# Kernel optimization log

Measured on AMD Instinct MI355X. Metric: run time of the kernel, lower is better.

The kernel has to match this reference:

```python
import jax, jax.numpy as jnp
import numpy as np
import math

N, C_IN, H, W = 8, 256, 64, 64
C_ATT, C_OUT = 128, 256
BN_EPS = 1e-5


def conv_bn_relu(x, w, gamma, beta, mean, var):
    # 1x1 conv (no bias) + BatchNorm (eval mode) + ReLU
    y = jnp.einsum('oc,nchw->nohw', w, x)
    inv = gamma / jnp.sqrt(var + BN_EPS)
    y = y * inv[None, :, None, None] + (beta - mean * inv)[None, :, None, None]
    return jax.nn.relu(y)


def setup_inputs() -> dict:
    key = jax.random.key(0)
    ks = jax.random.split(key, 12)
    x = jax.random.normal(ks[0], (N, C_IN, H, W), dtype=jnp.float32)
    mask = jnp.ones((N, 1, H, W), dtype=jnp.float32)
    reduc_w = jax.random.normal(ks[1], (C_OUT, C_IN), dtype=jnp.float32) * (1.0 / math.sqrt(C_IN))
    reduc_gamma = jnp.ones((C_OUT,), dtype=jnp.float32)
    reduc_beta = jnp.zeros((C_OUT,), dtype=jnp.float32)
    reduc_mean = jax.random.normal(ks[2], (C_OUT,), dtype=jnp.float32) * 0.1
    reduc_var = jax.random.uniform(ks[3], (C_OUT,), dtype=jnp.float32) + 0.5
    att_w = jax.random.normal(ks[4], (C_ATT, C_IN), dtype=jnp.float32) * (1.0 / math.sqrt(C_IN))
    att_gamma = jnp.ones((C_ATT,), dtype=jnp.float32)
    att_beta = jnp.zeros((C_ATT,), dtype=jnp.float32)
    att_mean = jax.random.normal(ks[5], (C_ATT,), dtype=jnp.float32) * 0.1
    att_var = jax.random.uniform(ks[6], (C_ATT,), dtype=jnp.float32) + 0.5
    return {
        'x': x, 'mask': mask,
        'reduc_w': reduc_w, 'reduc_gamma': reduc_gamma, 'reduc_beta': reduc_beta,
        'reduc_mean': reduc_mean, 'reduc_var': reduc_var,
        'att_w': att_w, 'att_gamma': att_gamma, 'att_beta': att_beta,
        'att_mean': att_mean, 'att_var': att_var,
    }


def reference(x, mask, reduc_w, reduc_gamma, reduc_beta, reduc_mean, reduc_var,
              att_w, att_gamma, att_beta, att_mean, att_var):
    n, _, h, w = x.shape
    x_feat = conv_bn_relu(x, reduc_w, reduc_gamma, reduc_beta, reduc_mean, reduc_var)   # [n,C_OUT,h,w]
    x_atten = conv_bn_relu(x, att_w, att_gamma, att_beta, att_mean, att_var)            # [n,C_ATT,h,w]
    c = x_atten.shape[1]
    q = x_atten.reshape(n, c, h * w)                                                    # [n,c,HW]
    # energy[n,i,j] = sum_c q[n,c,i]*q[n,c,j] / (1e-8 + sqrt(c))
    energy = jnp.einsum('nci,ncj->nij', q, q) / (1e-8 + math.sqrt(c))
    energy = energy + (mask.reshape(n, 1, h * w) - 1.0) * 1e8
    weight = jax.nn.softmax(energy, axis=2)                                             # [n,HW,HW]
    feat = x_feat.reshape(n, x_feat.shape[1], h * w)                                    # [n,C_OUT,HW]
    out = jnp.einsum('nij,ncj->nci', weight, feat)                                      # [n,C_OUT,HW]
    out = out.reshape(n, feat.shape[1], h, w)
    out = out * mask
    return out
```

## Files before the change

### kernel.cpp

```cpp
#include <hip/hip_runtime.h>
#include <cstdint>
#include <cstddef>

#define NB 8
#define CIN 256
#define HWX 4096
#define CF 256
#define CA 128
#define CT 384

typedef __attribute__((ext_vector_type(8))) _Float16 half8;
typedef __attribute__((ext_vector_type(8))) short short8;
typedef __attribute__((ext_vector_type(4))) float f32x4;
typedef __attribute__((ext_vector_type(4))) unsigned int u32x4;

#define OFF_WH   0
#define OFF_BIAS (CT*CIN*2)
#define OFF_FEAT (OFF_BIAS + CT*4)
#define OFF_Q    (OFF_FEAT + NB*CF*HWX*2)
#define OFF_NORM (OFF_Q + NB*HWX*CA*2)
#define OFF_G    (OFF_NORM + NB*HWX*4)

__device__ inline unsigned short f16_bits(float f) {
  _Float16 h = (_Float16)f;
  return __builtin_bit_cast(unsigned short, h);
}
__device__ inline half8 ld_half8(const unsigned short* p) {
  short8 r = *(const short8*)p;
  return __builtin_bit_cast(half8, r);
}

__device__ inline void g2l16(const void* g, void* l) {
  __builtin_amdgcn_global_load_lds(
      (const __attribute__((address_space(1))) unsigned int*)g,
      (__attribute__((address_space(3))) unsigned int*)l, 16, 0, 0);
}

__global__ __launch_bounds__(256) void fold_bn_k(
    const float* __restrict__ rw, const float* __restrict__ rg,
    const float* __restrict__ rb, const float* __restrict__ rm, const float* __restrict__ rv,
    const float* __restrict__ aw, const float* __restrict__ ag,
    const float* __restrict__ ab2, const float* __restrict__ am, const float* __restrict__ av,
    unsigned short* __restrict__ wh, float* __restrict__ bias, unsigned* __restrict__ Gmax) {
  int o = blockIdx.x, k = threadIdx.x;
  if (o == 0 && k < NB) Gmax[k] = 0u;
  const float* wsrc; float g, b, m, v;
  if (o < CF) { wsrc = rw + (size_t)o*CIN; g = rg[o]; b = rb[o]; m = rm[o]; v = rv[o]; }
  else { int oa = o - CF; wsrc = aw + (size_t)oa*CIN; g = ag[oa]; b = ab2[oa]; m = am[oa]; v = av[oa]; }
  float inv = g / sqrtf(v + 1e-5f);
  wh[(size_t)o*CIN + k] = f16_bits(wsrc[k] * inv);
  if (k == 0) bias[o] = b - m*inv;
}

__global__ __launch_bounds__(256, 2) void conv_k(
    const float* __restrict__ x, const unsigned short* __restrict__ wh,
    const float* __restrict__ bias, unsigned short* __restrict__ feat,
    unsigned short* __restrict__ q, float* __restrict__ normq,
    unsigned* __restrict__ Gmax) {
  __shared__ unsigned short sBuf[18432];
  __shared__ unsigned short sQr[64*136];
  int b = blockIdx.x;
  int n = b & 7, pt0 = b >> 3;
  int p0 = pt0 * 64;
  int t = threadIdx.x;
  int w = t >> 6, lane = t & 63, quad = lane >> 4, col = lane & 15;
  const float* xn = x + (size_t)n*CIN*HWX;

  #pragma unroll
  for (int pass=0; pass<8; pass++) {
    int idx = pass*256 + t;
    int kp = idx >> 4, pq = idx & 15;
    f32x4 a = *(const f32x4*)(xn + (size_t)(2*kp)*HWX + p0 + pq*4);
    f32x4 c = *(const f32x4*)(xn + (size_t)(2*kp+1)*HWX + p0 + pq*4);
    #pragma unroll
    for (int j=0;j<4;j++) {
      int pos = pq*4 + j;
      unsigned dd = (unsigned)f16_bits(a[j]) | ((unsigned)f16_bits(c[j]) << 16);
      *(unsigned*)&sBuf[pos*264 + kp*2] = dd;
    }
  }
  __syncthreads();

  f32x4 fzero = {0.f,0.f,0.f,0.f};
  f32x4 acc[4][6];
  #pragma unroll
  for (int pt=0;pt<4;pt++)
    #pragma unroll
    for (int ot=0;ot<6;ot++) acc[pt][ot] = fzero;

  #pragma unroll
  for (int ks=0; ks<8; ks++) {
    half8 B6[6];
    #pragma unroll
    for (int ot=0;ot<6;ot++)
      B6[ot] = ld_half8(wh + (size_t)(w*96 + ot*16 + col)*CIN + ks*32 + quad*8);
    half8 A4[4];
    #pragma unroll
    for (int pt=0;pt<4;pt++)
      A4[pt] = ld_half8(&sBuf[(pt*16+col)*264 + ks*32 + quad*8]);
    #pragma unroll
    for (int pt=0;pt<4;pt++)
      #pragma unroll
      for (int ot=0;ot<6;ot++)
        acc[pt][ot] = __builtin_amdgcn_mfma_f32_16x16x32_f16(A4[pt], B6[ot], acc[pt][ot], 0, 0, 0);
  }
  __syncthreads();

  float bv[6];
  #pragma unroll
  for (int ot=0;ot<6;ot++) bv[ot] = bias[w*96 + ot*16 + col];
  #pragma unroll
  for (int pt=0;pt<4;pt++)
    #pragma unroll
    for (int ot=0;ot<6;ot++) {
      int oc = w*96 + ot*16 + col;
      #pragma unroll
      for (int r=0;r<4;r++) {
        float v = fmaxf(acc[pt][ot][r] + bv[ot], 0.f);
        int pos = pt*16 + quad*4 + r;
        if (oc < CF) sBuf[oc*72 + pos] = f16_bits(v);
        else         sQr[pos*136 + (oc - CF)] = f16_bits(v);
      }
    }
  __syncthreads();

  {
    const unsigned short* src = &sBuf[t*72];
    unsigned short* dst = feat + (size_t)n*CF*HWX + (size_t)t*HWX + p0;
    #pragma unroll
    for (int s=0;s<8;s++)
      *(u32x4*)(dst + s*8) = *(const u32x4*)(src + s*8);
  }
  {
    int pos = t >> 2, seg = t & 3;
    const unsigned short* src = &sQr[pos*136 + seg*32];
    unsigned short* dst = q + ((size_t)n*HWX + p0 + pos)*CA + seg*32;
    float s2 = 0.f;
    #pragma unroll
    for (int u=0;u<4;u++) {
      short8 v = *(const short8*)(src + u*8);
      *(short8*)(dst + u*8) = v;
      half8 h = __builtin_bit_cast(half8, v);
      #pragma unroll
      for (int e=0;e<8;e++) { float fe = (float)h[e]; s2 += fe*fe; }
    }
    s2 += __shfl_xor(s2, 1, 64);
    s2 += __shfl_xor(s2, 2, 64);
    if (seg == 0) {
      float nv = sqrtf(s2);
      normq[(size_t)n*HWX + p0 + pos] = nv;
      atomicMax(Gmax + n, __float_as_uint(nv));
    }
  }
}

__global__ __launch_bounds__(512, 4) void flash_k(
    const unsigned short* __restrict__ q, const unsigned short* __restrict__ feat,
    const float* __restrict__ mask, const float* __restrict__ normq,
    const unsigned* __restrict__ Gmax, float* __restrict__ out) {
  __shared__ alignas(16) unsigned short sQ[64*128];
  __shared__ alignas(16) unsigned short sP[64][72];
  __shared__ float sM[64];
  __shared__ float sL[2][64];
  int b = blockIdx.x;
  int n = b & 7, it = b >> 3;
  int i0 = it * 64;
  int t = threadIdx.x;
  int w = t >> 6, lane = t & 63, quad = lane >> 4, col = lane & 15;
  int wq = w & 3, wh = w >> 2;
  const unsigned short* q_n = q + (size_t)n*HWX*CA;
  const unsigned short* f_n = feat + (size_t)n*CF*HWX;
  const float* m_n = mask + (size_t)n*HWX;
  const int rloc = (t >> 4) & 31, oct16 = t & 15;
  const float inv_s = 1.0f/(1e-8f + sqrtf(128.0f));

  auto stage_Q = [&](int j0) {
    #pragma unroll
    for (int c=0;c<2;c++) {
      int row = c*32 + rloc;
      int og = oct16 ^ (row & 15);
      g2l16(q_n + (size_t)(j0+row)*CA + og*8, &sQ[(size_t)row*128 + oct16*8]);
    }
    if (t < 16) g2l16(m_n + j0 + t*4, &sM[t*4]);
  };

  half8 ah[4];
  {
    int arow = i0 + wq*16 + col;
    #pragma unroll
    for (int ks=0; ks<4; ks++)
      ah[ks] = ld_half8(q_n + (size_t)arow*CA + ks*32 + quad*8);
  }
  float Gn = __uint_as_float(Gmax[n]);
  float cvals[4];
  #pragma unroll
  for (int r=0;r<4;r++)
    cvals[r] = normq[(size_t)n*HWX + i0 + wq*16 + quad*4 + r] * Gn * inv_s - 5.0f;

  f32x4 fzero = {0.f,0.f,0.f,0.f};
  f32x4 o[4][2];
  #pragma unroll
  for (int ig=0;ig<4;ig++) { o[ig][0] = fzero; o[ig][1] = fzero; }
  float lrun[4] = {0.f,0.f,0.f,0.f};

  stage_Q(0);
  for (int ji = 0; ji < 64; ji++) {
    int j0 = ji*64;
    __syncthreads();

    half8 bF[2][2];
    #pragma unroll
    for (int ks2=0;ks2<2;ks2++)
      #pragma unroll
      for (int ct=0;ct<2;ct++) {
        int c = w*32 + ct*16 + col;
        bF[ks2][ct] = ld_half8(f_n + (size_t)c*HWX + j0 + ks2*32 + quad*8);
      }

    f32x4 s[2];
    s[0] = fzero; s[1] = fzero;
    #pragma unroll
    for (int jt=0;jt<2;jt++) {
      int rowj = wh*32 + jt*16 + col;
      #pragma unroll
      for (int ks=0; ks<4; ks++) {
        int slot = (ks*4 + quad) ^ (rowj & 15);
        half8 bq = ld_half8(&sQ[rowj*128 + slot*8]);
        s[jt] = __builtin_amdgcn_mfma_f32_16x16x32_f16(ah[ks], bq, s[jt], 0, 0, 0);
      }
    }

    #pragma unroll
    for (int jt=0;jt<2;jt++) {
      float mj = (sM[wh*32 + jt*16 + col] - 1.f) * 1e8f;
      #pragma unroll
      for (int r=0;r<4;r++) {
        float p = __expf(s[jt][r]*inv_s + mj - cvals[r]);
        lrun[r] += p;
        sP[wq*16 + quad*4 + r][wh*32 + jt*16 + col] = f16_bits(p);
      }
    }

    __syncthreads();
    if (ji + 1 < 64) stage_Q(j0+64);

    #pragma unroll
    for (int ks2=0; ks2<2; ks2++) {
      half8 aP[4];
      #pragma unroll
      for (int ig=0;ig<4;ig++)
        aP[ig] = ld_half8(&sP[ig*16 + col][ks2*32 + quad*8]);
      #pragma unroll
      for (int ct=0;ct<2;ct++)
        #pragma unroll
        for (int ig=0;ig<4;ig++)
          o[ig][ct] = __builtin_amdgcn_mfma_f32_16x16x32_f16(aP[ig], bF[ks2][ct], o[ig][ct], 0, 0, 0);
    }
  }

  #pragma unroll
  for (int r=0;r<4;r++) {
    float ss = lrun[r];
    ss += __shfl_xor(ss, 1, 64);
    ss += __shfl_xor(ss, 2, 64);
    ss += __shfl_xor(ss, 4, 64);
    ss += __shfl_xor(ss, 8, 64);
    lrun[r] = ss;
  }
  #pragma unroll
  for (int r=0;r<4;r++)
    if (col == 0) sL[wh][wq*16 + quad*4 + r] = lrun[r];
  __syncthreads();
  #pragma unroll
  for (int ig=0;ig<4;ig++) {
    int base = ig*16 + quad*4;
    f32x4 l0 = *(const f32x4*)&sL[0][base];
    f32x4 l1 = *(const f32x4*)&sL[1][base];
    f32x4 mv = *(const f32x4*)(m_n + i0 + base);
    f32x4 minv;
    #pragma unroll
    for (int r=0;r<4;r++) minv[r] = mv[r] / (l0[r] + l1[r]);
    #pragma unroll
    for (int ct=0;ct<2;ct++) {
      int c = w*32 + ct*16 + col;
      f32x4 v;
      #pragma unroll
      for (int r=0;r<4;r++) v[r] = o[ig][ct][r] * minv[r];
      *(f32x4*)(out + ((size_t)n*CF + c)*HWX + i0 + base) = v;
    }
  }
}

extern "C" void kernel_launch(void* const* d_in, const int* in_sizes, int n_in,
                              void* d_out, int out_size, void* d_ws, size_t ws_size,
                              hipStream_t stream) {
  const float* x    = (const float*)d_in[0];
  const float* mask = (const float*)d_in[1];
  const float* rw   = (const float*)d_in[2];
  const float* rg   = (const float*)d_in[3];
  const float* rb   = (const float*)d_in[4];
  const float* rm   = (const float*)d_in[5];
  const float* rv   = (const float*)d_in[6];
  const float* aw   = (const float*)d_in[7];
  const float* ag   = (const float*)d_in[8];
  const float* ab   = (const float*)d_in[9];
  const float* am   = (const float*)d_in[10];
  const float* av   = (const float*)d_in[11];
  float* out = (float*)d_out;
  char* ws = (char*)d_ws;
  unsigned short* wh = (unsigned short*)(ws + OFF_WH);
  float* bias = (float*)(ws + OFF_BIAS);
  unsigned short* feat = (unsigned short*)(ws + OFF_FEAT);
  unsigned short* q    = (unsigned short*)(ws + OFF_Q);
  float* normq = (float*)(ws + OFF_NORM);
  unsigned* Gmax = (unsigned*)(ws + OFF_G);

  hipLaunchKernelGGL(fold_bn_k, dim3(CT), dim3(CIN), 0, stream,
                     rw, rg, rb, rm, rv, aw, ag, ab, am, av, wh, bias, Gmax);
  hipLaunchKernelGGL(conv_k, dim3(512), dim3(256), 0, stream,
                     x, wh, bias, feat, q, normq, Gmax);
  hipLaunchKernelGGL(flash_k, dim3(512), dim3(512), 0, stream,
                     q, feat, mask, normq, Gmax, out);
}
```

Measured before the change: 295.2 us.

## Double-buffer flash loop so softmax overlaps PV; shrink conv tiles

The attention kernel now keeps two Q/P/mask buffers and a software-pipelined loop. The QK^T plus exp for tile j+1 is issued alongside the PV MFMAs for tile j, with one barrier per tile instead of two. The conv kernel moves to 32-pixel tiles with twice the blocks and higher occupancy, writes feat straight from registers, and does a wave-level max reduction before a single atomic per wave. The cost is double the LDS in the flash kernel, which may hurt occupancy, plus narrower 8-byte feat stores.

```diff
diff --git a/kernel.cpp b/kernel.cpp
--- a/kernel.cpp
+++ b/kernel.cpp
@@ -13,6 +13,7 @@
 typedef __attribute__((ext_vector_type(8))) short short8;
 typedef __attribute__((ext_vector_type(4))) float f32x4;
 typedef __attribute__((ext_vector_type(4))) unsigned int u32x4;
+typedef __attribute__((ext_vector_type(2))) unsigned int u32x2;
 
 #define OFF_WH   0
 #define OFF_BIAS (CT*CIN*2)
@@ -52,39 +53,39 @@
   if (k == 0) bias[o] = b - m*inv;
 }
 
-__global__ __launch_bounds__(256, 2) void conv_k(
+__global__ __launch_bounds__(256, 4) void conv_k(
     const float* __restrict__ x, const unsigned short* __restrict__ wh,
     const float* __restrict__ bias, unsigned short* __restrict__ feat,
     unsigned short* __restrict__ q, float* __restrict__ normq,
     unsigned* __restrict__ Gmax) {
-  __shared__ unsigned short sBuf[18432];
-  __shared__ unsigned short sQr[64*136];
+  __shared__ unsigned short sX[32*264];
+  __shared__ unsigned short sQr[32][136];
   int b = blockIdx.x;
   int n = b & 7, pt0 = b >> 3;
-  int p0 = pt0 * 64;
+  int p0 = pt0 * 32;
   int t = threadIdx.x;
   int w = t >> 6, lane = t & 63, quad = lane >> 4, col = lane & 15;
   const float* xn = x + (size_t)n*CIN*HWX;
 
   #pragma unroll
-  for (int pass=0; pass<8; pass++) {
+  for (int pass=0; pass<4; pass++) {
     int idx = pass*256 + t;
-    int kp = idx >> 4, pq = idx & 15;
-    f32x4 a = *(const f32x4*)(xn + (size_t)(2*kp)*HWX + p0 + pq*4);
-    f32x4 c = *(const f32x4*)(xn + (size_t)(2*kp+1)*HWX + p0 + pq*4);
+    int kp = idx >> 3, pl = idx & 7;
+    f32x4 a = *(const f32x4*)(xn + (size_t)(2*kp)*HWX + p0 + pl*4);
+    f32x4 c = *(const f32x4*)(xn + (size_t)(2*kp+1)*HWX + p0 + pl*4);
     #pragma unroll
     for (int j=0;j<4;j++) {
-      int pos = pq*4 + j;
+      int pos = pl*4 + j;
       unsigned dd = (unsigned)f16_bits(a[j]) | ((unsigned)f16_bits(c[j]) << 16);
-      *(unsigned*)&sBuf[pos*264 + kp*2] = dd;
+      *(unsigned*)&sX[pos*264 + kp*2] = dd;
     }
   }
   __syncthreads();
 
   f32x4 fzero = {0.f,0.f,0.f,0.f};
-  f32x4 acc[4][6];
-  #pragma unroll
-  for (int pt=0;pt<4;pt++)
+  f32x4 acc[2][6];
+  #pragma unroll
+  for (int pt=0;pt<2;pt++)
     #pragma unroll
     for (int ot=0;ot<6;ot++) acc[pt][ot] = fzero;
 
@@ -94,46 +95,44 @@
     #pragma unroll
     for (int ot=0;ot<6;ot++)
       B6[ot] = ld_half8(wh + (size_t)(w*96 + ot*16 + col)*CIN + ks*32 + quad*8);
-    half8 A4[4];
-    #pragma unroll
-    for (int pt=0;pt<4;pt++)
-      A4[pt] = ld_half8(&sBuf[(pt*16+col)*264 + ks*32 + quad*8]);
-    #pragma unroll
-    for (int pt=0;pt<4;pt++)
+    half8 A2[2];
+    #pragma unroll
+    for (int pt=0;pt<2;pt++)
+      A2[pt] = ld_half8(&sX[(pt*16+col)*264 + ks*32 + quad*8]);
+    #pragma unroll
+    for (int pt=0;pt<2;pt++)
       #pragma unroll
       for (int ot=0;ot<6;ot++)
-        acc[pt][ot] = __builtin_amdgcn_mfma_f32_16x16x32_f16(A4[pt], B6[ot], acc[pt][ot], 0, 0, 0);
-  }
-  __syncthreads();
+        acc[pt][ot] = __builtin_amdgcn_mfma_f32_16x16x32_f16(A2[pt], B6[ot], acc[pt][ot], 0, 0, 0);
+  }
 
   float bv[6];
   #pragma unroll
   for (int ot=0;ot<6;ot++) bv[ot] = bias[w*96 + ot*16 + col];
   #pragma unroll
-  for (int pt=0;pt<4;pt++)
+  for (int pt=0;pt<2;pt++)
     #pragma unroll
     for (int ot=0;ot<6;ot++) {
       int oc = w*96 + ot*16 + col;
-      #pragma unroll
-      for (int r=0;r<4;r++) {
-        float v = fmaxf(acc[pt][ot][r] + bv[ot], 0.f);
-        int pos = pt*16 + quad*4 + r;
-        if (oc < CF) sBuf[oc*72 + pos] = f16_bits(v);
-        else         sQr[pos*136 + (oc - CF)] = f16_bits(v);
+      alignas(8) unsigned short u4[4];
+      #pragma unroll
+      for (int r=0;r<4;r++)
+        u4[r] = f16_bits(fmaxf(acc[pt][ot][r] + bv[ot], 0.f));
+      if (oc < CF) {
+        *(u32x2*)(feat + (size_t)n*CF*HWX + (size_t)oc*HWX + p0 + pt*16 + quad*4) =
+            *(const u32x2*)u4;
+      } else {
+        int cc = oc - CF;
+        #pragma unroll
+        for (int r=0;r<4;r++)
+          sQr[pt*16 + quad*4 + r][cc] = u4[r];
       }
     }
   __syncthreads();
 
-  {
-    const unsigned short* src = &sBuf[t*72];
-    unsigned short* dst = feat + (size_t)n*CF*HWX + (size_t)t*HWX + p0;
-    #pragma unroll
-    for (int s=0;s<8;s++)
-      *(u32x4*)(dst + s*8) = *(const u32x4*)(src + s*8);
-  }
-  {
+  if (t < 128) {
     int pos = t >> 2, seg = t & 3;
-    const unsigned short* src = &sQr[pos*136 + seg*32];
+    const unsigned short* src = &sQr[pos][seg*32];
     unsigned short* dst = q + ((size_t)n*HWX + p0 + pos)*CA + seg*32;
     float s2 = 0.f;
     #pragma unroll
@@ -146,11 +145,13 @@
     }
     s2 += __shfl_xor(s2, 1, 64);
     s2 += __shfl_xor(s2, 2, 64);
-    if (seg == 0) {
-      float nv = sqrtf(s2);
-      normq[(size_t)n*HWX + p0 + pos] = nv;
-      atomicMax(Gmax + n, __float_as_uint(nv));
-    }
+    if (seg == 0) normq[(size_t)n*HWX + p0 + pos] = sqrtf(s2);
+    float mx = s2;
+    mx = fmaxf(mx, __shfl_xor(mx, 4, 64));
+    mx = fmaxf(mx, __shfl_xor(mx, 8, 64));
+    mx = fmaxf(mx, __shfl_xor(mx, 16, 64));
+    mx = fmaxf(mx, __shfl_xor(mx, 32, 64));
+    if (lane == 0) atomicMax(Gmax + n, __float_as_uint(sqrtf(mx)));
   }
 }
 
@@ -158,9 +159,9 @@
     const unsigned short* __restrict__ q, const unsigned short* __restrict__ feat,
     const float* __restrict__ mask, const float* __restrict__ normq,
     const unsigned* __restrict__ Gmax, float* __restrict__ out) {
-  __shared__ alignas(16) unsigned short sQ[64*128];
-  __shared__ alignas(16) unsigned short sP[64][72];
-  __shared__ float sM[64];
+  __shared__ alignas(16) unsigned short sQ[2][64*128];
+  __shared__ alignas(16) unsigned short sP[2][64][72];
+  __shared__ float sM[2][64];
   __shared__ float sL[2][64];
   int b = blockIdx.x;
   int n = b & 7, it = b >> 3;
@@ -174,41 +175,18 @@
   const int rloc = (t >> 4) & 31, oct16 = t & 15;
   const float inv_s = 1.0f/(1e-8f + sqrtf(128.0f));
 
-  auto stage_Q = [&](int j0) {
+  auto stage_Q = [&](int ji, int buf) {
+    int j0 = ji*64;
     #pragma unroll
     for (int c=0;c<2;c++) {
       int row = c*32 + rloc;
       int og = oct16 ^ (row & 15);
-      g2l16(q_n + (size_t)(j0+row)*CA + og*8, &sQ[(size_t)row*128 + oct16*8]);
-    }
-    if (t < 16) g2l16(m_n + j0 + t*4, &sM[t*4]);
+      g2l16(q_n + (size_t)(j0+row)*CA + og*8, &sQ[buf][(size_t)row*128 + oct16*8]);
+    }
+    if (t < 16) g2l16(m_n + j0 + t*4, &sM[buf][t*4]);
   };
-
-  half8 ah[4];
-  {
-    int arow = i0 + wq*16 + col;
-    #pragma unroll
-    for (int ks=0; ks<4; ks++)
-      ah[ks] = ld_half8(q_n + (size_t)arow*CA + ks*32 + quad*8);
-  }
-  float Gn = __uint_as_float(Gmax[n]);
-  float cvals[4];
-  #pragma unroll
-  for (int r=0;r<4;r++)
-    cvals[r] = normq[(size_t)n*HWX + i0 + wq*16 + quad*4 + r] * Gn * inv_s - 5.0f;
-
-  f32x4 fzero = {0.f,0.f,0.f,0.f};
-  f32x4 o[4][2];
-  #pragma unroll
-  for (int ig=0;ig<4;ig++) { o[ig][0] = fzero; o[ig][1] = fzero; }
-  float lrun[4] = {0.f,0.f,0.f,0.f};
-
-  stage_Q(0);
-  for (int ji = 0; ji < 64; ji++) {
+  auto load_bF = [&](int ji, half8 (&bF)[2][2]) {
     int j0 = ji*64;
-    __syncthreads();
-
-    half8 bF[2][2];
     #pragma unroll
     for (int ks2=0;ks2<2;ks2++)
       #pragma unroll
@@ -216,7 +194,28 @@
         int c = w*32 + ct*16 + col;
         bF[ks2][ct] = ld_half8(f_n + (size_t)c*HWX + j0 + ks2*32 + quad*8);
       }
-
+  };
+
+  half8 ah[4];
+  {
+    int arow = i0 + wq*16 + col;
+    #pragma unroll
+    for (int ks=0; ks<4; ks++)
+      ah[ks] = ld_half8(q_n + (size_t)arow*CA + ks*32 + quad*8);
+  }
+  float Gn = __uint_as_float(Gmax[n]);
+  float cvals[4];
+  #pragma unroll
+  for (int r=0;r<4;r++)
+    cvals[r] = normq[(size_t)n*HWX + i0 + wq*16 + quad*4 + r] * Gn * inv_s - 5.0f;
+
+  f32x4 fzero = {0.f,0.f,0.f,0.f};
+  f32x4 o[4][2];
+  #pragma unroll
+  for (int ig=0;ig<4;ig++) { o[ig][0] = fzero; o[ig][1] = fzero; }
+  float lrun[4] = {0.f,0.f,0.f,0.f};
+
+  auto qk_softmax = [&](int buf) {
     f32x4 s[2];
     s[0] = fzero; s[1] = fzero;
     #pragma unroll
@@ -225,38 +224,63 @@
       #pragma unroll
       for (int ks=0; ks<4; ks++) {
         int slot = (ks*4 + quad) ^ (rowj & 15);
-        half8 bq = ld_half8(&sQ[rowj*128 + slot*8]);
+        half8 bq = ld_half8(&sQ[buf][rowj*128 + slot*8]);
         s[jt] = __builtin_amdgcn_mfma_f32_16x16x32_f16(ah[ks], bq, s[jt], 0, 0, 0);
       }
     }
-
     #pragma unroll
     for (int jt=0;jt<2;jt++) {
-      float mj = (sM[wh*32 + jt*16 + col] - 1.f) * 1e8f;
+      float mj = (sM[buf][wh*32 + jt*16 + col] - 1.f) * 1e8f;
       #pragma unroll
       for (int r=0;r<4;r++) {
         float p = __expf(s[jt][r]*inv_s + mj - cvals[r]);
         lrun[r] += p;
-        sP[wq*16 + quad*4 + r][wh*32 + jt*16 + col] = f16_bits(p);
+        sP[buf][wq*16 + quad*4 + r][wh*32 + jt*16 + col] = f16_bits(p);
       }
     }
-
-    __syncthreads();
-    if (ji + 1 < 64) stage_Q(j0+64);
-
+  };
+  auto do_PV = [&](int buf, half8 (&bF)[2][2]) {
     #pragma unroll
     for (int ks2=0; ks2<2; ks2++) {
       half8 aP[4];
       #pragma unroll
       for (int ig=0;ig<4;ig++)
-        aP[ig] = ld_half8(&sP[ig*16 + col][ks2*32 + quad*8]);
+        aP[ig] = ld_half8(&sP[buf][ig*16 + col][ks2*32 + quad*8]);
       #pragma unroll
       for (int ct=0;ct<2;ct++)
         #pragma unroll
         for (int ig=0;ig<4;ig++)
           o[ig][ct] = __builtin_amdgcn_mfma_f32_16x16x32_f16(aP[ig], bF[ks2][ct], o[ig][ct], 0, 0, 0);
     }
-  }
+  };
+
+  half8 bFa[2][2], bFb[2][2];
+  stage_Q(0, 0);
+  __syncthreads();
+  stage_Q(1, 1);
+  load_bF(0, bFa);
+  qk_softmax(0);
+
+  #pragma unroll 1
+  for (int jj = 0; jj < 31; jj++) {
+    int ji = 2*jj + 1;
+    __syncthreads();
+    stage_Q(ji+1, 0);
+    load_bF(ji, bFb);
+    qk_softmax(1);
+    do_PV(0, bFa);
+    __syncthreads();
+    stage_Q(ji+2, 1);
+    load_bF(ji+1, bFa);
+    qk_softmax(0);
+    do_PV(1, bFb);
+  }
+  __syncthreads();
+  load_bF(63, bFb);
+  qk_softmax(1);
+  do_PV(0, bFa);
+  __syncthreads();
+  do_PV(1, bFb);
 
   #pragma unroll
   for (int r=0;r<4;r++) {
@@ -317,7 +341,7 @@
 
   hipLaunchKernelGGL(fold_bn_k, dim3(CT), dim3(CIN), 0, stream,
                      rw, rg, rb, rm, rv, aw, ag, ab, am, av, wh, bias, Gmax);
-  hipLaunchKernelGGL(conv_k, dim3(512), dim3(256), 0, stream,
+  hipLaunchKernelGGL(conv_k, dim3(1024), dim3(256), 0, stream,
                      x, wh, bias, feat, q, normq, Gmax);
   hipLaunchKernelGGL(flash_k, dim3(512), dim3(512), 0, stream,
                      q, feat, mask, normq, Gmax, out);
```

After: 317.1 us. +7.4%, slower.

## Double conv block threads, swizzle LDS, and widen flash key tile to 128

Applied to the files above, without the earlier changes.

The conv kernel now runs 512 threads, with each wave handling 48 output channels. It uses an XOR-swizzled LDS layout for the input tile and writes feat straight to global memory instead of staging it. The per-row atomicMax on Gmax becomes a wave-level max reduction followed by one atomic per wave. The flash kernel processes 128 key columns per iteration instead of 64, halving the loop trips and barriers at the cost of more LDS and registers. This may reduce occupancy and changes how the feat loads are scheduled.

```diff
diff --git a/kernel.cpp b/kernel.cpp
--- a/kernel.cpp
+++ b/kernel.cpp
@@ -13,6 +13,7 @@
 typedef __attribute__((ext_vector_type(8))) short short8;
 typedef __attribute__((ext_vector_type(4))) float f32x4;
 typedef __attribute__((ext_vector_type(4))) unsigned int u32x4;
+typedef __attribute__((ext_vector_type(2))) unsigned int u32x2;
 
 #define OFF_WH   0
 #define OFF_BIAS (CT*CIN*2)
@@ -52,13 +53,13 @@
   if (k == 0) bias[o] = b - m*inv;
 }
 
-__global__ __launch_bounds__(256, 2) void conv_k(
+__global__ __launch_bounds__(512, 4) void conv_k(
     const float* __restrict__ x, const unsigned short* __restrict__ wh,
     const float* __restrict__ bias, unsigned short* __restrict__ feat,
     unsigned short* __restrict__ q, float* __restrict__ normq,
     unsigned* __restrict__ Gmax) {
-  __shared__ unsigned short sBuf[18432];
-  __shared__ unsigned short sQr[64*136];
+  __shared__ unsigned short sX[64*256];
+  unsigned short (*sQr)[136] = (unsigned short(*)[136])sX;
   int b = blockIdx.x;
   int n = b & 7, pt0 = b >> 3;
   int p0 = pt0 * 64;
@@ -67,73 +68,76 @@
   const float* xn = x + (size_t)n*CIN*HWX;
 
   #pragma unroll
-  for (int pass=0; pass<8; pass++) {
-    int idx = pass*256 + t;
-    int kp = idx >> 4, pq = idx & 15;
-    f32x4 a = *(const f32x4*)(xn + (size_t)(2*kp)*HWX + p0 + pq*4);
-    f32x4 c = *(const f32x4*)(xn + (size_t)(2*kp+1)*HWX + p0 + pq*4);
+  for (int pass=0; pass<4; pass++) {
+    int idx = pass*512 + t;
+    int kp = idx >> 4, c4 = idx & 15;
+    f32x4 a = *(const f32x4*)(xn + (size_t)(2*kp)*HWX + p0 + c4*4);
+    f32x4 c = *(const f32x4*)(xn + (size_t)(2*kp+1)*HWX + p0 + c4*4);
+    int unit = kp >> 2, off = kp & 3;
     #pragma unroll
     for (int j=0;j<4;j++) {
-      int pos = pq*4 + j;
+      int pos = c4*4 + j;
       unsigned dd = (unsigned)f16_bits(a[j]) | ((unsigned)f16_bits(c[j]) << 16);
-      *(unsigned*)&sBuf[pos*264 + kp*2] = dd;
+      *(unsigned*)&sX[pos*256 + ((unit ^ (pos & 31)) << 3) + off*2] = dd;
     }
   }
   __syncthreads();
 
   f32x4 fzero = {0.f,0.f,0.f,0.f};
-  f32x4 acc[4][6];
+  f32x4 acc[4][3];
   #pragma unroll
   for (int pt=0;pt<4;pt++)
     #pragma unroll
-    for (int ot=0;ot<6;ot++) acc[pt][ot] = fzero;
-
+    for (int ot=0;ot<3;ot++) acc[pt][ot] = fzero;
+
+  int ocb = w*48;
   #pragma unroll
   for (int ks=0; ks<8; ks++) {
-    half8 B6[6];
-    #pragma unroll
-    for (int ot=0;ot<6;ot++)
-      B6[ot] = ld_half8(wh + (size_t)(w*96 + ot*16 + col)*CIN + ks*32 + quad*8);
+    half8 B3[3];
+    #pragma unroll
+    for (int ot=0;ot<3;ot++)
+      B3[ot] = ld_half8(wh + (size_t)(ocb + ot*16 + col)*CIN + ks*32 + quad*8);
     half8 A4[4];
     #pragma unroll
+    for (int pt=0;pt<4;pt++) {
+      int pos = pt*16 + col;
+      A4[pt] = ld_half8(&sX[pos*256 + (((ks*4 + quad) ^ (pos & 31)) << 3)]);
+    }
+    #pragma unroll
     for (int pt=0;pt<4;pt++)
-      A4[pt] = ld_half8(&sBuf[(pt*16+col)*264 + ks*32 + quad*8]);
-    #pragma unroll
-    for (int pt=0;pt<4;pt++)
-      #pragma unroll
-      for (int ot=0;ot<6;ot++)
-        acc[pt][ot] = __builtin_amdgcn_mfma_f32_16x16x32_f16(A4[pt], B6[ot], acc[pt][ot], 0, 0, 0);
+      #pragma unroll
+      for (int ot=0;ot<3;ot++)
+        acc[pt][ot] = __builtin_amdgcn_mfma_f32_16x16x32_f16(A4[pt], B3[ot], acc[pt][ot], 0, 0, 0);
   }
   __syncthreads();
 
-  float bv[6];
-  #pragma unroll
-  for (int ot=0;ot<6;ot++) bv[ot] = bias[w*96 + ot*16 + col];
+  float bv[3];
+  #pragma unroll
+  for (int ot=0;ot<3;ot++) bv[ot] = bias[ocb + ot*16 + col];
   #pragma unroll
   for (int pt=0;pt<4;pt++)
     #pragma unroll
-    for (int ot=0;ot<6;ot++) {
-      int oc = w*96 + ot*16 + col;
-      #pragma unroll
-      for (int r=0;r<4;r++) {
-        float v = fmaxf(acc[pt][ot][r] + bv[ot], 0.f);
-        int pos = pt*16 + quad*4 + r;
-        if (oc < CF) sBuf[oc*72 + pos] = f16_bits(v);
-        else         sQr[pos*136 + (oc - CF)] = f16_bits(v);
+    for (int ot=0;ot<3;ot++) {
+      int oc = ocb + ot*16 + col;
+      alignas(8) unsigned short u4[4];
+      #pragma unroll
+      for (int r=0;r<4;r++)
+        u4[r] = f16_bits(fmaxf(acc[pt][ot][r] + bv[ot], 0.f));
+      if (oc < CF) {
+        *(u32x2*)(feat + (size_t)n*CF*HWX + (size_t)oc*HWX + p0 + pt*16 + quad*4) =
+            *(const u32x2*)u4;
+      } else {
+        int cc = oc - CF;
+        #pragma unroll
+        for (int r=0;r<4;r++)
+          sQr[pt*16 + quad*4 + r][cc] = u4[r];
       }
     }
   __syncthreads();
 
-  {
-    const unsigned short* src = &sBuf[t*72];
-    unsigned short* dst = feat + (size_t)n*CF*HWX + (size_t)t*HWX + p0;
-    #pragma unroll
-    for (int s=0;s<8;s++)
-      *(u32x4*)(dst + s*8) = *(const u32x4*)(src + s*8);
-  }
-  {
+  if (t < 256) {
     int pos = t >> 2, seg = t & 3;
-    const unsigned short* src = &sQr[pos*136 + seg*32];
+    const unsigned short* src = &sQr[pos][seg*32];
     unsigned short* dst = q + ((size_t)n*HWX + p0 + pos)*CA + seg*32;
     float s2 = 0.f;
     #pragma unroll
@@ -146,11 +150,13 @@
     }
     s2 += __shfl_xor(s2, 1, 64);
     s2 += __shfl_xor(s2, 2, 64);
-    if (seg == 0) {
-      float nv = sqrtf(s2);
-      normq[(size_t)n*HWX + p0 + pos] = nv;
-      atomicMax(Gmax + n, __float_as_uint(nv));
-    }
+    if (seg == 0) normq[(size_t)n*HWX + p0 + pos] = sqrtf(s2);
+    float mx = s2;
+    mx = fmaxf(mx, __shfl_xor(mx, 4, 64));
+    mx = fmaxf(mx, __shfl_xor(mx, 8, 64));
+    mx = fmaxf(mx, __shfl_xor(mx, 16, 64));
+    mx = fmaxf(mx, __shfl_xor(mx, 32, 64));
+    if (lane == 0) atomicMax(Gmax + n, __float_as_uint(sqrtf(mx)));
   }
 }
 
@@ -158,9 +164,9 @@
     const unsigned short* __restrict__ q, const unsigned short* __restrict__ feat,
     const float* __restrict__ mask, const float* __restrict__ normq,
     const unsigned* __restrict__ Gmax, float* __restrict__ out) {
-  __shared__ alignas(16) unsigned short sQ[64*128];
-  __shared__ alignas(16) unsigned short sP[64][72];
-  __shared__ float sM[64];
+  __shared__ alignas(16) unsigned short sQ[128*128];
+  __shared__ alignas(16) unsigned short sP[64][136];
+  __shared__ float sM[128];
   __shared__ float sL[2][64];
   int b = blockIdx.x;
   int n = b & 7, it = b >> 3;
@@ -171,17 +177,17 @@
   const unsigned short* q_n = q + (size_t)n*HWX*CA;
   const unsigned short* f_n = feat + (size_t)n*CF*HWX;
   const float* m_n = mask + (size_t)n*HWX;
-  const int rloc = (t >> 4) & 31, oct16 = t & 15;
+  const int rloc = t >> 4 & 31, oct16 = t & 15;
   const float inv_s = 1.0f/(1e-8f + sqrtf(128.0f));
 
   auto stage_Q = [&](int j0) {
     #pragma unroll
-    for (int c=0;c<2;c++) {
+    for (int c=0;c<4;c++) {
       int row = c*32 + rloc;
       int og = oct16 ^ (row & 15);
       g2l16(q_n + (size_t)(j0+row)*CA + og*8, &sQ[(size_t)row*128 + oct16*8]);
     }
-    if (t < 16) g2l16(m_n + j0 + t*4, &sM[t*4]);
+    if (t < 32) g2l16(m_n + j0 + t*4, &sM[t*4]);
   };
 
   half8 ah[4];
@@ -204,24 +210,26 @@
   float lrun[4] = {0.f,0.f,0.f,0.f};
 
   stage_Q(0);
-  for (int ji = 0; ji < 64; ji++) {
-    int j0 = ji*64;
+  #pragma unroll 1
+  for (int ji = 0; ji < 32; ji++) {
+    int j0 = ji*128;
     __syncthreads();
 
-    half8 bF[2][2];
+    half8 bF01[2][2];
     #pragma unroll
     for (int ks2=0;ks2<2;ks2++)
       #pragma unroll
       for (int ct=0;ct<2;ct++) {
         int c = w*32 + ct*16 + col;
-        bF[ks2][ct] = ld_half8(f_n + (size_t)c*HWX + j0 + ks2*32 + quad*8);
-      }
-
-    f32x4 s[2];
-    s[0] = fzero; s[1] = fzero;
-    #pragma unroll
-    for (int jt=0;jt<2;jt++) {
-      int rowj = wh*32 + jt*16 + col;
+        bF01[ks2][ct] = ld_half8(f_n + (size_t)c*HWX + j0 + ks2*32 + quad*8);
+      }
+
+    f32x4 s[4];
+    #pragma unroll
+    for (int jt=0;jt<4;jt++) s[jt] = fzero;
+    #pragma unroll
+    for (int jt=0;jt<4;jt++) {
+      int rowj = wh*64 + jt*16 + col;
       #pragma unroll
       for (int ks=0; ks<4; ks++) {
         int slot = (ks*4 + quad) ^ (rowj & 15);
@@ -231,30 +239,40 @@
     }
 
     #pragma unroll
-    for (int jt=0;jt<2;jt++) {
-      float mj = (sM[wh*32 + jt*16 + col] - 1.f) * 1e8f;
+    for (int jt=0;jt<4;jt++) {
+      float mj = (sM[wh*64 + jt*16 + col] - 1.f) * 1e8f;
       #pragma unroll
       for (int r=0;r<4;r++) {
         float p = __expf(s[jt][r]*inv_s + mj - cvals[r]);
         lrun[r] += p;
-        sP[wq*16 + quad*4 + r][wh*32 + jt*16 + col] = f16_bits(p);
+        sP[wq*16 + quad*4 + r][wh*64 + jt*16 + col] = f16_bits(p);
       }
     }
 
     __syncthreads();
-    if (ji + 1 < 64) stage_Q(j0+64);
-
-    #pragma unroll
-    for (int ks2=0; ks2<2; ks2++) {
+    if (ji + 1 < 32) stage_Q(j0+128);
+
+    half8 bF23[2][2];
+    #pragma unroll
+    for (int ks2=0;ks2<2;ks2++)
+      #pragma unroll
+      for (int ct=0;ct<2;ct++) {
+        int c = w*32 + ct*16 + col;
+        bF23[ks2][ct] = ld_half8(f_n + (size_t)c*HWX + j0 + (ks2+2)*32 + quad*8);
+      }
+    #pragma unroll
+    for (int ks2=0; ks2<4; ks2++) {
       half8 aP[4];
       #pragma unroll
       for (int ig=0;ig<4;ig++)
         aP[ig] = ld_half8(&sP[ig*16 + col][ks2*32 + quad*8]);
       #pragma unroll
-      for (int ct=0;ct<2;ct++)
+      for (int ct=0;ct<2;ct++) {
+        half8 bF = (ks2 < 2) ? bF01[ks2][ct] : bF23[ks2-2][ct];
         #pragma unroll
         for (int ig=0;ig<4;ig++)
-          o[ig][ct] = __builtin_amdgcn_mfma_f32_16x16x32_f16(aP[ig], bF[ks2][ct], o[ig][ct], 0, 0, 0);
+          o[ig][ct] = __builtin_amdgcn_mfma_f32_16x16x32_f16(aP[ig], bF, o[ig][ct], 0, 0, 0);
+      }
     }
   }
 
@@ -317,7 +335,7 @@
 
   hipLaunchKernelGGL(fold_bn_k, dim3(CT), dim3(CIN), 0, stream,
                      rw, rg, rb, rm, rv, aw, ag, ab, am, av, wh, bias, Gmax);
-  hipLaunchKernelGGL(conv_k, dim3(512), dim3(256), 0, stream,
+  hipLaunchKernelGGL(conv_k, dim3(512), dim3(512), 0, stream,
                      x, wh, bias, feat, q, normq, Gmax);
   hipLaunchKernelGGL(flash_k, dim3(512), dim3(512), 0, stream,
                      q, feat, mask, normq, Gmax, out);
```

Measured after the change: 293.9 us. Within noise of the previous version (-0.4%).
